# Kernel tuning notes

Hardware: AMD Instinct MI355X
Metric: run time of the kernel (lower is better)

## Reference

```python
import jax, jax.numpy as jnp
import numpy as np

B, H, W = 1, 352, 1216
T = 6          # prop_time
CG = 8         # guidance channels per step
K = 9          # 3x3 propagation kernel


def _conv(x, w, b, pad, groups=1):
    out = jax.lax.conv_general_dilated(
        x, w, (1, 1), [(pad, pad), (pad, pad)],
        dimension_numbers=('NCHW', 'OIHW', 'NCHW'),
        feature_group_count=groups)
    return out if b is None else out + b[None, :, None, None]


def setup_inputs() -> dict:
    key = jax.random.key(0)
    ks = iter(jax.random.split(key, 32))
    def r(shape, s=0.1):
        return jax.random.normal(next(ks), shape, jnp.float32) * s
    return dict(
        feat_init=r((B, 1, H, W), 1.0),
        guidance=r((B, T * CG, H, W), 1.0),
        attn=r((B, 16, H, W), 1.0),
        feat_fix=r((B, 1, H, W), 1.0),
        aff_w_w=r((T, K, CG, 3, 3)), aff_w_b=r((T, K)),
        aff_o_w=r((T, 2 * (K - 1), CG, 3, 3)), aff_o_b=r((T, 2 * (K - 1))),
        proj_w=r((6, 3, 1, 1)),
        bn_gamma=jnp.ones((6,), jnp.float32), bn_beta=jnp.zeros((6,), jnp.float32),
        bn_mean=jnp.zeros((6,), jnp.float32), bn_var=jnp.ones((6,), jnp.float32),
        lsk0_w=r((22, 1, 1, 1)), lsk0_b=r((22,)),
        lsks_w=r((22, 1, 3, 3)), lsks_b=r((22,)),
        lsk1_w=r((11, 22, 1, 1)), lsk1_b=r((11,)),
        lsk2_w=r((11, 22, 1, 1)), lsk2_b=r((11,)),
        lsksq_w=r((2, 2, 3, 3)), lsksq_b=r((2,)),
        lskc_w=r((3, 11, 1, 1)), lskc_b=r((3,)),
    )


def _forward(feat_init, guidance, attn,
             aff_w_w, aff_w_b, aff_o_w, aff_o_b,
             proj_w, bn_gamma, bn_beta, bn_mean, bn_var,
             lsk0_w, lsk0_b, lsks_w, lsks_b, lsk1_w, lsk1_b,
             lsk2_w, lsk2_b, lsksq_w, lsksq_b, lskc_w, lskc_b):
    Bs, _, Hs, Ws = feat_init.shape
    # split guidance into T chunks of CG channels -> (T,B,CG,H,W)
    g = guidance.reshape(Bs, T, CG, Hs, Ws).transpose(1, 0, 2, 3, 4)

    def aff_fn(g_t, ww, wb, ow, ob):
        w = jax.nn.sigmoid(_conv(g_t, ww, wb, 1))              # (B,9,H,W)
        w = w / (w.sum(1, keepdims=True) + 1e-8)
        o = _conv(g_t, ow, ob, 1).reshape(Bs, K - 1, 2, Hs, Ws)
        zero = jnp.zeros((Bs, 1, 2, Hs, Ws), o.dtype)          # reference pixel
        o = jnp.concatenate([o[:, :4], zero, o[:, 4:]], 1).reshape(Bs, 2 * K, Hs, Ws)
        return o, w

    offs, affs = jax.vmap(aff_fn)(g, aff_w_w, aff_w_b, aff_o_w, aff_o_b)

    # modulated deformable conv, weight = ones(1,1,3,3), bias = 0, stride=1, pad=1
    ky = (jnp.repeat(jnp.arange(3), 3) - 1).astype(feat_init.dtype)  # (9,)
    kx = (jnp.tile(jnp.arange(3), 3) - 1).astype(feat_init.dtype)
    yy = jnp.arange(Hs, dtype=feat_init.dtype)
    xx = jnp.arange(Ws, dtype=feat_init.dtype)
    bidx = jnp.arange(Bs)[:, None, None, None]

    def dcn(feat, off, aff):
        img = feat[:, 0]                                       # (B,H,W)
        ys = yy[None, None, :, None] + ky[None, :, None, None] + off[:, 0::2]
        xs = xx[None, None, None, :] + kx[None, :, None, None] + off[:, 1::2]
        y0 = jnp.floor(ys); x0 = jnp.floor(xs)
        wy = ys - y0; wx = xs - x0
        y0i = y0.astype(jnp.int32); x0i = x0.astype(jnp.int32)
        def g4(yi, xi):
            valid = (yi >= 0) & (yi < Hs) & (xi >= 0) & (xi < Ws)
            v = img[bidx, jnp.clip(yi, 0, Hs - 1), jnp.clip(xi, 0, Ws - 1)]
            return v * valid.astype(v.dtype)
        samp = (g4(y0i, x0i) * (1 - wy) * (1 - wx)
                + g4(y0i, x0i + 1) * (1 - wy) * wx
                + g4(y0i + 1, x0i) * wy * (1 - wx)
                + g4(y0i + 1, x0i + 1) * wy * wx)
        return (aff * samp).sum(1)[:, None]                    # (B,1,H,W)

    def step(f, ox):
        o, a = ox
        fn = dcn(f, o, a)
        return fn, fn

    _, feats = jax.lax.scan(step, feat_init.astype(jnp.float32), (offs, affs))

    # combine(list_feat[3:6], attn)
    x3 = jnp.concatenate([feats[3], feats[4], feats[5]], 1)    # (B,3,H,W)
    sf = _conv(x3, proj_w, None, 0)                            # conv 3->6, no bias
    sf = (sf - bn_mean[None, :, None, None]) * jax.lax.rsqrt(bn_var + 1e-5)[None, :, None, None] \
         * bn_gamma[None, :, None, None] + bn_beta[None, :, None, None]
    sf = jnp.where(sf >= 0, sf, 0.2 * sf)                      # LeakyReLU(0.2)
    x22 = jnp.concatenate([attn, sf], 1)                       # (B,22,H,W)

    a1 = _conv(x22, lsk0_w, lsk0_b, 0, 22)                     # depthwise 1x1
    a2 = _conv(a1, lsks_w, lsks_b, 1, 22)                      # depthwise 3x3
    a1 = _conv(a1, lsk1_w, lsk1_b, 0)                          # 22->11
    a2 = _conv(a2, lsk2_w, lsk2_b, 0)                          # 22->11
    cat = jnp.concatenate([a1, a2], 1)
    agg = jnp.concatenate([cat.mean(1, keepdims=True), cat.max(1, keepdims=True)], 1)
    sig = jax.nn.sigmoid(_conv(agg, lsksq_w, lsksq_b, 1))
    at = a1 * sig[:, 0:1] + a2 * sig[:, 1:2]
    at = _conv(at, lskc_w, lskc_b, 0)                          # 11->3
    return (x3 * at).sum(1, keepdims=True)                     # (B,1,H,W)


def reference(feat_init, guidance, attn, feat_fix,
              aff_w_w, aff_w_b, aff_o_w, aff_o_b,
              proj_w, bn_gamma, bn_beta, bn_mean, bn_var,
              lsk0_w, lsk0_b, lsks_w, lsks_b, lsk1_w, lsk1_b,
              lsk2_w, lsk2_b, lsksq_w, lsksq_b, lskc_w, lskc_b):
    # feat_fix only feeds an unused mask path (if False branch) in the original
    return _forward(feat_init, guidance, attn,
                    aff_w_w, aff_w_b, aff_o_w, aff_o_b,
                    proj_w, bn_gamma, bn_beta, bn_mean, bn_var,
                    lsk0_w, lsk0_b, lsks_w, lsks_b, lsk1_w, lsk1_b,
                    lsk2_w, lsk2_b, lsksq_w, lsksq_b, lskc_w, lskc_b)
```

## Files before the change

### kernel.cpp

```cpp
#include <hip/hip_runtime.h>
#include <hip/hip_bf16.h>

#define HH 352
#define WW 1216
#define HWSZ (HH * WW)
#define TT 6

#define WS_CW   16
#define WS_TW   11008
#define WS_FB   12032

typedef __attribute__((ext_vector_type(4))) float f32x4;
typedef __attribute__((ext_vector_type(8))) short s16x8;
union FU { unsigned int u[4]; s16x8 v; };

__device__ inline float ld_in(const void* p, long long i, int bf) {
    return bf ? __bfloat162float(((const __hip_bfloat16*)p)[i]) : ((const float*)p)[i];
}

__device__ inline unsigned int bfsplit_pack(float v) {
    unsigned int uv = __float_as_uint(v);
    unsigned int h = (uv + 0x7FFFu + ((uv >> 16) & 1u)) >> 16;
    float hf = __uint_as_float(h << 16);
    float r = v - hf;
    unsigned int ur = __float_as_uint(r);
    unsigned int l = (ur + 0x7FFFu + ((ur >> 16) & 1u)) >> 16;
    return (h & 0xFFFFu) | (l << 16);
}

__device__ inline int detect_mode(const void* guid) {
    const unsigned int* u = (const unsigned int*)guid;
    int cnt = 0;
    for (int i = 0; i < 128; ++i) {
        unsigned int lo = u[i] & 0xFFFFu;
        int e = (int)((lo >> 7) & 0xFF);
        if (e >= 110 && e <= 140) cnt++;
    }
    return (cnt >= 96) ? 1 : 0;
}

__global__ void prep_small(const void* guid,
                           const void* aww, const void* awb, const void* aow, const void* aob,
                           const void* projw, const void* bng, const void* bnb,
                           const void* bnm, const void* bnv,
                           const void* l0w, const void* l0b, const void* lsw, const void* lsb,
                           const void* l1w, const void* l1b, const void* l2w, const void* l2b,
                           const void* sqw, const void* sqb, const void* lcw, const void* lcb,
                           float* ws) {
    __shared__ int smode;
    if (threadIdx.x == 0) {
        int mode = detect_mode(guid);
        smode = mode;
        if (blockIdx.x == 0) *(int*)ws = mode;
    }
    __syncthreads();
    const int bf = smode;
    const int tid = blockIdx.x * blockDim.x + threadIdx.x;
    const int stp = gridDim.x * blockDim.x;
    float* cw = ws + WS_CW;
    for (int idx = tid; idx < TT * 9 * 72; idx += stp) {
        int t = idx / 648; int r = idx % 648;
        int co = r / 72; int ci = (r % 72) / 9; int tap = r % 9;
        cw[t * 1825 + 25 + co * 72 + ci * 9 + tap] = ld_in(aww, idx, bf);
    }
    for (int idx = tid; idx < TT * 16 * 72; idx += stp) {
        int t = idx / 1152; int r = idx % 1152;
        int co = r / 72; int ci = (r % 72) / 9; int tap = r % 9;
        cw[t * 1825 + 25 + (9 + co) * 72 + ci * 9 + tap] = ld_in(aow, idx, bf);
    }
    for (int idx = tid; idx < TT * 9; idx += stp)
        cw[(idx / 9) * 1825 + (idx % 9)] = ld_in(awb, idx, bf);
    for (int idx = tid; idx < TT * 16; idx += stp)
        cw[(idx / 16) * 1825 + 9 + (idx % 16)] = ld_in(aob, idx, bf);

    float* tw = ws + WS_TW;
    for (int i = tid; i < 18; i += stp) tw[i] = ld_in(projw, i, bf);
    for (int i = tid; i < 6; i += stp) {
        float sc = ld_in(bng, i, bf) * rsqrtf(ld_in(bnv, i, bf) + 1e-5f);
        tw[18 + i] = sc;
        tw[24 + i] = ld_in(bnb, i, bf) - ld_in(bnm, i, bf) * sc;
    }
    for (int i = tid; i < 22;  i += stp) tw[32  + i] = ld_in(l0w, i, bf);
    for (int i = tid; i < 22;  i += stp) tw[54  + i] = ld_in(l0b, i, bf);
    for (int i = tid; i < 198; i += stp) tw[76  + i] = ld_in(lsw, i, bf);
    for (int i = tid; i < 22;  i += stp) tw[274 + i] = ld_in(lsb, i, bf);
    for (int i = tid; i < 242; i += stp) tw[296 + i] = ld_in(l1w, i, bf);
    for (int i = tid; i < 11;  i += stp) tw[538 + i] = ld_in(l1b, i, bf);
    for (int i = tid; i < 242; i += stp) tw[549 + i] = ld_in(l2w, i, bf);
    for (int i = tid; i < 11;  i += stp) tw[791 + i] = ld_in(l2b, i, bf);
    for (int i = tid; i < 36;  i += stp) tw[802 + i] = ld_in(sqw, i, bf);
    for (int i = tid; i < 2;   i += stp) tw[838 + i] = ld_in(sqb, i, bf);
    for (int i = tid; i < 33;  i += stp) tw[840 + i] = ld_in(lcw, i, bf);
    for (int i = tid; i < 3;   i += stp) tw[873 + i] = ld_in(lcb, i, bf);
}

__global__ void prep_feat(const void* __restrict__ feat_init, const int* __restrict__ flagp,
                          float* __restrict__ dst) {
    int bf = *flagp;
    int i = blockIdx.x * 256 + threadIdx.x;
    if (i < HWSZ) dst[i] = ld_in(feat_init, i, bf);
}

__device__ inline float samp(const float* __restrict__ src, int y, int x) {
    bool valid = (y >= 0) & (y < HH) & (x >= 0) & (x < WW);
    int yc = min(max(y, 0), HH - 1);
    int xc = min(max(x, 0), WW - 1);
    float v = src[yc * WW + xc];
    return valid ? v : 0.0f;
}

__global__ __launch_bounds__(256) void dcn_fused(
        const void* __restrict__ guid, const int* __restrict__ flagp,
        const float* __restrict__ wts,
        const float* __restrict__ src, float* __restrict__ dst, int t) {
    __shared__ unsigned int hal[8][10][36];
    __shared__ float outb[4][64][27];
    const int bf = *flagp;
    const int bx = blockIdx.x % 38, by = blockIdx.x / 38;
    const int x0 = bx * 32, y0 = by * 8;
    for (int idx = threadIdx.x; idx < 8 * 360; idx += 256) {
        int ci = idx / 360; int r = (idx % 360) / 36; int c = idx % 36;
        int gy = y0 - 1 + r, gx = x0 - 1 + c;
        float v = 0.f;
        if (c < 34 && gy >= 0 && gy < HH && gx >= 0 && gx < WW)
            v = ld_in(guid, (long long)(t * 8 + ci) * HWSZ + gy * WW + gx, bf);
        hal[ci][r][c] = bfsplit_pack(v);
    }
    const int lane = threadIdx.x & 63;
    const int wave = threadIdx.x >> 6;
    const int col = lane & 15, g = lane >> 4;

    FU Bh[2][3], Bl[2][3];
#pragma unroll
    for (int Nt = 0; Nt < 2; ++Nt)
#pragma unroll
    for (int c = 0; c < 3; ++c) {
        unsigned short eh[8], el[8];
#pragma unroll
        for (int j = 0; j < 8; ++j) {
            int ci = 2 * g + (j >> 2), dx = j & 3;
            int cc = Nt * 16 + col;
            float w = 0.f;
            if (cc < 25 && dx < 3) w = wts[25 + cc * 72 + ci * 9 + c * 3 + dx];
            unsigned int pk = bfsplit_pack(w);
            eh[j] = (unsigned short)(pk & 0xFFFFu);
            el[j] = (unsigned short)(pk >> 16);
        }
#pragma unroll
        for (int q = 0; q < 4; ++q) {
            Bh[Nt][c].u[q] = (unsigned int)eh[2*q] | ((unsigned int)eh[2*q+1] << 16);
            Bl[Nt][c].u[q] = (unsigned int)el[2*q] | ((unsigned int)el[2*q+1] << 16);
        }
    }
    __syncthreads();

    const float* bias = wts;
#pragma unroll
    for (int m = 0; m < 4; ++m) {
        const int M = wave * 4 + m;
        const int py = M >> 1;
        const int pxx = (M & 1) * 16 + col;
        FU Ah[3], Al[3];
#pragma unroll
        for (int c = 0; c < 3; ++c) {
            const unsigned int* r0 = &hal[2 * g][py + c][pxx];
            const unsigned int* r1 = &hal[2 * g + 1][py + c][pxx];
            unsigned int q0 = r0[0], q1 = r0[1], q2 = r0[2], q3 = r0[3];
            unsigned int q4 = r1[0], q5 = r1[1], q6 = r1[2], q7 = r1[3];
            Ah[c].u[0] = __builtin_amdgcn_perm(q1, q0, 0x05040100u);
            Ah[c].u[1] = __builtin_amdgcn_perm(q3, q2, 0x05040100u);
            Ah[c].u[2] = __builtin_amdgcn_perm(q5, q4, 0x05040100u);
            Ah[c].u[3] = __builtin_amdgcn_perm(q7, q6, 0x05040100u);
            Al[c].u[0] = __builtin_amdgcn_perm(q1, q0, 0x07060302u);
            Al[c].u[1] = __builtin_amdgcn_perm(q3, q2, 0x07060302u);
            Al[c].u[2] = __builtin_amdgcn_perm(q5, q4, 0x07060302u);
            Al[c].u[3] = __builtin_amdgcn_perm(q7, q6, 0x07060302u);
        }
#pragma unroll
        for (int Nt = 0; Nt < 2; ++Nt) {
            f32x4 acc = {0.f, 0.f, 0.f, 0.f};
#pragma unroll
            for (int c = 0; c < 3; ++c) {
                acc = __builtin_amdgcn_mfma_f32_16x16x32_bf16(Ah[c].v, Bh[Nt][c].v, acc, 0, 0, 0);
                acc = __builtin_amdgcn_mfma_f32_16x16x32_bf16(Al[c].v, Bh[Nt][c].v, acc, 0, 0, 0);
                acc = __builtin_amdgcn_mfma_f32_16x16x32_bf16(Ah[c].v, Bl[Nt][c].v, acc, 0, 0, 0);
            }
            const int co = Nt * 16 + col;
            if (co < 25) {
                float bs = bias[co];
#pragma unroll
                for (int r = 0; r < 4; ++r)
                    outb[wave][m * 16 + g * 4 + r][co] = acc[r] + bs;
            }
        }
    }
    __syncthreads();
    {
        const int pl = lane;
        const int Ml = pl >> 4, rd = pl & 15;
        const int M = wave * 4 + Ml;
        const int py = M >> 1;
        const int pxx = (M & 1) * 16 + rd;
        const int gy = y0 + py, gx = x0 + pxx;
        float v[25];
#pragma unroll
        for (int c = 0; c < 25; ++c) v[c] = outb[wave][pl][c];
        float w9[9], s = 0.f;
#pragma unroll
        for (int k = 0; k < 9; ++k) { w9[k] = 1.f / (1.f + __expf(-v[k])); s += w9[k]; }
        const float inv = 1.f / (s + 1e-8f);
        float out = 0.f;
#pragma unroll
        for (int k = 0; k < 9; ++k) {
            float oy = 0.f, ox = 0.f;
            if (k != 4) {
                int kp = (k < 4) ? k : (k - 1);
                oy = v[9 + 2 * kp];
                ox = v[10 + 2 * kp];
            }
            float ys = (float)(gy + k / 3 - 1) + oy;
            float xs = (float)(gx + k % 3 - 1) + ox;
            float yf = floorf(ys), xf = floorf(xs);
            float wy = ys - yf, wx = xs - xf;
            int yi = (int)yf, xi = (int)xf;
            float v00 = samp(src, yi, xi);
            float v01 = samp(src, yi, xi + 1);
            float v10 = samp(src, yi + 1, xi);
            float v11 = samp(src, yi + 1, xi + 1);
            float sv = v00 * (1.f - wy) * (1.f - wx) + v01 * (1.f - wy) * wx
                     + v10 * wy * (1.f - wx) + v11 * wy * wx;
            out = fmaf(w9[k] * inv, sv, out);
        }
        dst[gy * WW + gx] = out;
    }
}

__global__ __launch_bounds__(256) void tail1(
        const void* __restrict__ attn, const int* __restrict__ flagp,
        const float* __restrict__ tw, const float* __restrict__ feats,
        float* __restrict__ a1) {
    const int bf = *flagp;
    const int p = blockIdx.x * 256 + threadIdx.x;
    float x3[3] = { feats[3 * HWSZ + p], feats[4 * HWSZ + p], feats[5 * HWSZ + p] };
    float sf[6];
#pragma unroll
    for (int j = 0; j < 6; ++j) {
        float v = tw[j * 3 + 0] * x3[0] + tw[j * 3 + 1] * x3[1] + tw[j * 3 + 2] * x3[2];
        v = v * tw[18 + j] + tw[24 + j];
        sf[j] = (v >= 0.0f) ? v : 0.2f * v;
    }
#pragma unroll
    for (int c = 0; c < 22; ++c) {
        float x = (c < 16) ? ld_in(attn, (long long)c * HWSZ + p, bf) : sf[c - 16];
        a1[c * HWSZ + p] = fmaf(x, tw[32 + c], tw[54 + c]);
    }
}

__global__ __launch_bounds__(256) void tail2(
        const float* __restrict__ tw, const float* __restrict__ a1,
        float* __restrict__ a11, float* __restrict__ a21, float* __restrict__ agg) {
    __shared__ float tile[10][34];
    const int bx = blockIdx.x % 38, by = blockIdx.x / 38;
    const int x0 = bx * 32, y0 = by * 8;
    const int lx = threadIdx.x % 32, ly = threadIdx.x / 32;
    float acc1[11], acc2[11];
#pragma unroll
    for (int j = 0; j < 11; ++j) { acc1[j] = tw[538 + j]; acc2[j] = tw[791 + j]; }
    for (int c = 0; c < 22; ++c) {
        __syncthreads();
        for (int idx = threadIdx.x; idx < 340; idx += 256) {
            int r = idx / 34, cc = idx % 34;
            int gy = y0 - 1 + r, gx = x0 - 1 + cc;
            tile[r][cc] = (gy >= 0 && gy < HH && gx >= 0 && gx < WW)
                          ? a1[c * HWSZ + gy * WW + gx] : 0.0f;
        }
        __syncthreads();
        float a1c = tile[ly + 1][lx + 1];
        float a2c = tw[274 + c];
#pragma unroll
        for (int dy = 0; dy < 3; ++dy)
#pragma unroll
            for (int dx = 0; dx < 3; ++dx)
                a2c = fmaf(tile[ly + dy][lx + dx], tw[76 + c * 9 + dy * 3 + dx], a2c);
#pragma unroll
        for (int j = 0; j < 11; ++j) {
            acc1[j] = fmaf(a1c, tw[296 + j * 22 + c], acc1[j]);
            acc2[j] = fmaf(a2c, tw[549 + j * 22 + c], acc2[j]);
        }
    }
    const int p = (y0 + ly) * WW + x0 + lx;
    float s = 0.0f, mx = -1e30f;
#pragma unroll
    for (int j = 0; j < 11; ++j) {
        a11[j * HWSZ + p] = acc1[j];
        a21[j * HWSZ + p] = acc2[j];
        s += acc1[j] + acc2[j];
        mx = fmaxf(mx, fmaxf(acc1[j], acc2[j]));
    }
    agg[p] = s * (1.0f / 22.0f);
    agg[HWSZ + p] = mx;
}

__global__ __launch_bounds__(256) void tail3(
        const int* __restrict__ flagp, const float* __restrict__ tw,
        const float* __restrict__ feats,
        const float* __restrict__ a11, const float* __restrict__ a21,
        const float* __restrict__ agg, void* __restrict__ out) {
    __shared__ float t0[10][34], t1[10][34];
    const int bx = blockIdx.x % 38, by = blockIdx.x / 38;
    const int x0 = bx * 32, y0 = by * 8;
    for (int idx = threadIdx.x; idx < 340; idx += 256) {
        int r = idx / 34, cc = idx % 34;
        int gy = y0 - 1 + r, gx = x0 - 1 + cc;
        bool ok = (gy >= 0 && gy < HH && gx >= 0 && gx < WW);
        t0[r][cc] = ok ? agg[gy * WW + gx] : 0.0f;
        t1[r][cc] = ok ? agg[HWSZ + gy * WW + gx] : 0.0f;
    }
    __syncthreads();
    const int lx = threadIdx.x % 32, ly = threadIdx.x / 32;
    float s0 = tw[838], s1 = tw[839];
#pragma unroll
    for (int dy = 0; dy < 3; ++dy)
#pragma unroll
        for (int dx = 0; dx < 3; ++dx) {
            float v0 = t0[ly + dy][lx + dx], v1 = t1[ly + dy][lx + dx];
            s0 = fmaf(v0, tw[802 + 0 * 18 + 0 * 9 + dy * 3 + dx], s0);
            s0 = fmaf(v1, tw[802 + 0 * 18 + 1 * 9 + dy * 3 + dx], s0);
            s1 = fmaf(v0, tw[802 + 1 * 18 + 0 * 9 + dy * 3 + dx], s1);
            s1 = fmaf(v1, tw[802 + 1 * 18 + 1 * 9 + dy * 3 + dx], s1);
        }
    float sg0 = 1.0f / (1.0f + __expf(-s0));
    float sg1 = 1.0f / (1.0f + __expf(-s1));
    const int p = (y0 + ly) * WW + x0 + lx;
    float at3[3] = { tw[873], tw[874], tw[875] };
#pragma unroll
    for (int j = 0; j < 11; ++j) {
        float at = a11[j * HWSZ + p] * sg0 + a21[j * HWSZ + p] * sg1;
#pragma unroll
        for (int i = 0; i < 3; ++i) at3[i] = fmaf(at, tw[840 + i * 11 + j], at3[i]);
    }
    float o = feats[3 * HWSZ + p] * at3[0] + feats[4 * HWSZ + p] * at3[1]
            + feats[5 * HWSZ + p] * at3[2];
    int bf = *flagp;
    if (bf) ((__hip_bfloat16*)out)[p] = __float2bfloat16(o);
    else    ((float*)out)[p] = o;
}

extern "C" void kernel_launch(void* const* d_in, const int* in_sizes, int n_in,
                              void* d_out, int out_size, void* d_ws, size_t ws_size,
                              hipStream_t stream) {
    (void)in_sizes; (void)n_in; (void)out_size; (void)ws_size;
    float* WSF = (float*)d_ws;
    const int* flagp = (const int*)d_ws;
    float* cw   = WSF + WS_CW;
    float* tw   = WSF + WS_TW;
    float* FB   = WSF + WS_FB;
    float* A1   = FB + 7 * HWSZ;
    float* A11  = A1 + 22 * HWSZ;
    float* A21  = A11 + 11 * HWSZ;
    float* AGG  = A21 + 11 * HWSZ;

    prep_small<<<32, 256, 0, stream>>>(d_in[1],
        d_in[4], d_in[5], d_in[6], d_in[7],
        d_in[8], d_in[9], d_in[10], d_in[11], d_in[12],
        d_in[13], d_in[14], d_in[15], d_in[16],
        d_in[17], d_in[18], d_in[19], d_in[20],
        d_in[21], d_in[22], d_in[23], d_in[24], WSF);
    prep_feat<<<(HWSZ + 255) / 256, 256, 0, stream>>>(d_in[0], flagp, FB + 6 * HWSZ);

    for (int t = 0; t < 6; ++t) {
        const float* src = (t == 0) ? (FB + 6 * HWSZ) : (FB + (t - 1) * HWSZ);
        dcn_fused<<<44 * 38, 256, 0, stream>>>(d_in[1], flagp, cw + t * 1825, src, FB + t * HWSZ, t);
    }
    tail1<<<HWSZ / 256, 256, 0, stream>>>(d_in[2], flagp, tw, FB, A1);
    tail2<<<44 * 38, 256, 0, stream>>>(tw, A1, A11, A21, AGG);
    tail3<<<44 * 38, 256, 0, stream>>>(flagp, tw, FB, A11, A21, AGG, d_out);
}
```

Measured before the change: 484.4 us.

## Fuse prep kernels, widen DCN to 512 threads, recompute LSK tail in shared memory

Merges the small-weight prep and the feat_init conversion into a single launch. The deformable conv kernel now runs 512 threads per block with one wave per row, and the two half-waves split the nine bilinear taps before combining them with a shuffle. The three tail kernels become two: tailA computes only the mean/max aggregate from a shared-memory tile, and tailB recomputes the 22-channel LSK activations instead of reading the 22+11+11 planes written to global memory earlier. This removes large global intermediates and one launch, at the cost of doing the LSK convolution twice and using more shared memory per block.

```diff
diff --git a/kernel.cpp b/kernel.cpp
--- a/kernel.cpp
+++ b/kernel.cpp
@@ -39,14 +39,15 @@
     return (cnt >= 96) ? 1 : 0;
 }
 
-__global__ void prep_small(const void* guid,
-                           const void* aww, const void* awb, const void* aow, const void* aob,
-                           const void* projw, const void* bng, const void* bnb,
-                           const void* bnm, const void* bnv,
-                           const void* l0w, const void* l0b, const void* lsw, const void* lsb,
-                           const void* l1w, const void* l1b, const void* l2w, const void* l2b,
-                           const void* sqw, const void* sqb, const void* lcw, const void* lcb,
-                           float* ws) {
+__global__ __launch_bounds__(256) void prep_all(
+        const void* feat_init, const void* guid,
+        const void* aww, const void* awb, const void* aow, const void* aob,
+        const void* projw, const void* bng, const void* bnb,
+        const void* bnm, const void* bnv,
+        const void* l0w, const void* l0b, const void* lsw, const void* lsb,
+        const void* l1w, const void* l1b, const void* l2w, const void* l2b,
+        const void* sqw, const void* sqb, const void* lcw, const void* lcb,
+        float* ws) {
     __shared__ int smode;
     if (threadIdx.x == 0) {
         int mode = detect_mode(guid);
@@ -55,8 +56,13 @@
     }
     __syncthreads();
     const int bf = smode;
-    const int tid = blockIdx.x * blockDim.x + threadIdx.x;
-    const int stp = gridDim.x * blockDim.x;
+    {
+        int i = blockIdx.x * 256 + threadIdx.x;
+        if (i < HWSZ) ws[WS_FB + 6 * HWSZ + i] = ld_in(feat_init, i, bf);
+    }
+    if (blockIdx.x >= 32) return;
+    const int tid = blockIdx.x * 256 + threadIdx.x;
+    const int stp = 32 * 256;
     float* cw = ws + WS_CW;
     for (int idx = tid; idx < TT * 9 * 72; idx += stp) {
         int t = idx / 648; int r = idx % 648;
@@ -94,13 +100,6 @@
     for (int i = tid; i < 3;   i += stp) tw[873 + i] = ld_in(lcb, i, bf);
 }
 
-__global__ void prep_feat(const void* __restrict__ feat_init, const int* __restrict__ flagp,
-                          float* __restrict__ dst) {
-    int bf = *flagp;
-    int i = blockIdx.x * 256 + threadIdx.x;
-    if (i < HWSZ) dst[i] = ld_in(feat_init, i, bf);
-}
-
 __device__ inline float samp(const float* __restrict__ src, int y, int x) {
     bool valid = (y >= 0) & (y < HH) & (x >= 0) & (x < WW);
     int yc = min(max(y, 0), HH - 1);
@@ -109,16 +108,16 @@
     return valid ? v : 0.0f;
 }
 
-__global__ __launch_bounds__(256) void dcn_fused(
+__global__ __launch_bounds__(512) void dcn_fused(
         const void* __restrict__ guid, const int* __restrict__ flagp,
         const float* __restrict__ wts,
         const float* __restrict__ src, float* __restrict__ dst, int t) {
     __shared__ unsigned int hal[8][10][36];
-    __shared__ float outb[4][64][27];
+    __shared__ float outb[8][32][26];
     const int bf = *flagp;
     const int bx = blockIdx.x % 38, by = blockIdx.x / 38;
     const int x0 = bx * 32, y0 = by * 8;
-    for (int idx = threadIdx.x; idx < 8 * 360; idx += 256) {
+    for (int idx = threadIdx.x; idx < 8 * 360; idx += 512) {
         int ci = idx / 360; int r = (idx % 360) / 36; int c = idx % 36;
         int gy = y0 - 1 + r, gx = x0 - 1 + c;
         float v = 0.f;
@@ -156,15 +155,13 @@
 
     const float* bias = wts;
 #pragma unroll
-    for (int m = 0; m < 4; ++m) {
-        const int M = wave * 4 + m;
-        const int py = M >> 1;
-        const int pxx = (M & 1) * 16 + col;
+    for (int m = 0; m < 2; ++m) {
+        const int pxx = m * 16 + col;
         FU Ah[3], Al[3];
 #pragma unroll
         for (int c = 0; c < 3; ++c) {
-            const unsigned int* r0 = &hal[2 * g][py + c][pxx];
-            const unsigned int* r1 = &hal[2 * g + 1][py + c][pxx];
+            const unsigned int* r0 = &hal[2 * g][wave + c][pxx];
+            const unsigned int* r1 = &hal[2 * g + 1][wave + c][pxx];
             unsigned int q0 = r0[0], q1 = r0[1], q2 = r0[2], q3 = r0[3];
             unsigned int q4 = r1[0], q5 = r1[1], q6 = r1[2], q7 = r1[3];
             Ah[c].u[0] = __builtin_amdgcn_perm(q1, q0, 0x05040100u);
@@ -194,32 +191,40 @@
             }
         }
     }
-    __syncthreads();
     {
-        const int pl = lane;
-        const int Ml = pl >> 4, rd = pl & 15;
-        const int M = wave * 4 + Ml;
-        const int py = M >> 1;
-        const int pxx = (M & 1) * 16 + rd;
-        const int gy = y0 + py, gx = x0 + pxx;
+        const int half = lane >> 5;
+        const int pxl = lane & 31;
+        const int gy = y0 + wave, gx = x0 + pxl;
         float v[25];
 #pragma unroll
-        for (int c = 0; c < 25; ++c) v[c] = outb[wave][pl][c];
+        for (int c = 0; c < 25; ++c) v[c] = outb[wave][pxl][c];
         float w9[9], s = 0.f;
 #pragma unroll
         for (int k = 0; k < 9; ++k) { w9[k] = 1.f / (1.f + __expf(-v[k])); s += w9[k]; }
         const float inv = 1.f / (s + 1e-8f);
         float out = 0.f;
 #pragma unroll
-        for (int k = 0; k < 9; ++k) {
-            float oy = 0.f, ox = 0.f;
-            if (k != 4) {
-                int kp = (k < 4) ? k : (k - 1);
-                oy = v[9 + 2 * kp];
-                ox = v[10 + 2 * kp];
-            }
-            float ys = (float)(gy + k / 3 - 1) + oy;
-            float xs = (float)(gx + k % 3 - 1) + ox;
+        for (int tp = 0; tp < 5; ++tp) {
+            const int ka = tp;
+            const int kb = tp + 5;
+            const bool vb = (kb < 9);
+            float wa = w9[ka] * inv;
+            float wb = vb ? w9[kb < 9 ? kb : 8] * inv : 0.f;
+            float w  = half ? wb : wa;
+            const int kpa = (ka < 4) ? ka : ka - 1;
+            const int kpb = vb ? ((kb < 4) ? kb : kb - 1) : 0;
+            float oya = (ka == 4) ? 0.f : v[9 + 2 * kpa];
+            float oxa = (ka == 4) ? 0.f : v[10 + 2 * kpa];
+            float oyb = vb ? v[9 + 2 * kpb] : 0.f;
+            float oxb = vb ? v[10 + 2 * kpb] : 0.f;
+            float oy = half ? oyb : oya;
+            float ox = half ? oxb : oxa;
+            const int dya = ka / 3 - 1, dxa = ka % 3 - 1;
+            const int dyb = vb ? kb / 3 - 1 : 0, dxb = vb ? kb % 3 - 1 : 0;
+            int dy = half ? dyb : dya;
+            int dx = half ? dxb : dxa;
+            float ys = (float)(gy + dy) + oy;
+            float xs = (float)(gx + dx) + ox;
             float yf = floorf(ys), xf = floorf(xs);
             float wy = ys - yf, wx = xs - xf;
             int yi = (int)yf, xi = (int)xf;
@@ -229,119 +234,140 @@
             float v11 = samp(src, yi + 1, xi + 1);
             float sv = v00 * (1.f - wy) * (1.f - wx) + v01 * (1.f - wy) * wx
                      + v10 * wy * (1.f - wx) + v11 * wy * wx;
-            out = fmaf(w9[k] * inv, sv, out);
-        }
-        dst[gy * WW + gx] = out;
-    }
-}
-
-__global__ __launch_bounds__(256) void tail1(
-        const void* __restrict__ attn, const int* __restrict__ flagp,
-        const float* __restrict__ tw, const float* __restrict__ feats,
-        float* __restrict__ a1) {
-    const int bf = *flagp;
-    const int p = blockIdx.x * 256 + threadIdx.x;
-    float x3[3] = { feats[3 * HWSZ + p], feats[4 * HWSZ + p], feats[5 * HWSZ + p] };
-    float sf[6];
-#pragma unroll
-    for (int j = 0; j < 6; ++j) {
-        float v = tw[j * 3 + 0] * x3[0] + tw[j * 3 + 1] * x3[1] + tw[j * 3 + 2] * x3[2];
-        v = v * tw[18 + j] + tw[24 + j];
-        sf[j] = (v >= 0.0f) ? v : 0.2f * v;
-    }
-#pragma unroll
-    for (int c = 0; c < 22; ++c) {
-        float x = (c < 16) ? ld_in(attn, (long long)c * HWSZ + p, bf) : sf[c - 16];
-        a1[c * HWSZ + p] = fmaf(x, tw[32 + c], tw[54 + c]);
-    }
-}
-
-__global__ __launch_bounds__(256) void tail2(
-        const float* __restrict__ tw, const float* __restrict__ a1,
-        float* __restrict__ a11, float* __restrict__ a21, float* __restrict__ agg) {
-    __shared__ float tile[10][34];
-    const int bx = blockIdx.x % 38, by = blockIdx.x / 38;
-    const int x0 = bx * 32, y0 = by * 8;
-    const int lx = threadIdx.x % 32, ly = threadIdx.x / 32;
-    float acc1[11], acc2[11];
+            out = fmaf(w, sv, out);
+        }
+        out += __shfl_xor(out, 32);
+        if (half == 0) dst[gy * WW + gx] = out;
+    }
+}
+
+__device__ inline void stage_a1_ft(const void* attn, int bf, const float* tw,
+                                   const float* feats, float (*a1t)[10][34],
+                                   float (*ft)[10][34], int x0, int y0) {
+    for (int idx = threadIdx.x; idx < 19 * 340; idx += 256) {
+        int plane = idx / 340; int r = (idx % 340) / 34; int cc = idx % 34;
+        int gy = y0 - 1 + r, gx = x0 - 1 + cc;
+        bool ok = (gy >= 0 && gy < HH && gx >= 0 && gx < WW);
+        if (plane < 16) {
+            float x = ok ? ld_in(attn, (long long)plane * HWSZ + gy * WW + gx, bf) : 0.f;
+            a1t[plane][r][cc] = ok ? fmaf(x, tw[32 + plane], tw[54 + plane]) : 0.f;
+        } else {
+            ft[plane - 16][r][cc] = ok ? feats[(long long)(3 + plane - 16) * HWSZ + gy * WW + gx] : 0.f;
+        }
+    }
+}
+
+__device__ inline void fill_sf(const float* tw, float (*a1t)[10][34],
+                               const float (*ft)[10][34], int x0, int y0) {
+    for (int idx = threadIdx.x; idx < 6 * 340; idx += 256) {
+        int j = idx / 340; int r = (idx % 340) / 34; int cc = idx % 34;
+        int gy = y0 - 1 + r, gx = x0 - 1 + cc;
+        bool ok = (gy >= 0 && gy < HH && gx >= 0 && gx < WW);
+        float o = 0.f;
+        if (ok) {
+            float f0 = ft[0][r][cc], f1 = ft[1][r][cc], f2 = ft[2][r][cc];
+            float v = tw[j * 3 + 0] * f0 + tw[j * 3 + 1] * f1 + tw[j * 3 + 2] * f2;
+            v = v * tw[18 + j] + tw[24 + j];
+            v = (v >= 0.f) ? v : 0.2f * v;
+            o = fmaf(v, tw[32 + 16 + j], tw[54 + 16 + j]);
+        }
+        a1t[16 + j][r][cc] = o;
+    }
+}
+
+__device__ inline void lsk_acc(const float (*a1t)[10][34], const float* tw,
+                               int lx, int ly, float* acc1, float* acc2) {
 #pragma unroll
     for (int j = 0; j < 11; ++j) { acc1[j] = tw[538 + j]; acc2[j] = tw[791 + j]; }
     for (int c = 0; c < 22; ++c) {
-        __syncthreads();
-        for (int idx = threadIdx.x; idx < 340; idx += 256) {
-            int r = idx / 34, cc = idx % 34;
-            int gy = y0 - 1 + r, gx = x0 - 1 + cc;
-            tile[r][cc] = (gy >= 0 && gy < HH && gx >= 0 && gx < WW)
-                          ? a1[c * HWSZ + gy * WW + gx] : 0.0f;
-        }
-        __syncthreads();
-        float a1c = tile[ly + 1][lx + 1];
+        float a1c = a1t[c][ly + 1][lx + 1];
         float a2c = tw[274 + c];
 #pragma unroll
         for (int dy = 0; dy < 3; ++dy)
 #pragma unroll
-            for (int dx = 0; dx < 3; ++dx)
-                a2c = fmaf(tile[ly + dy][lx + dx], tw[76 + c * 9 + dy * 3 + dx], a2c);
+        for (int dx = 0; dx < 3; ++dx)
+            a2c = fmaf(a1t[c][ly + dy][lx + dx], tw[76 + c * 9 + dy * 3 + dx], a2c);
 #pragma unroll
         for (int j = 0; j < 11; ++j) {
             acc1[j] = fmaf(a1c, tw[296 + j * 22 + c], acc1[j]);
             acc2[j] = fmaf(a2c, tw[549 + j * 22 + c], acc2[j]);
         }
     }
-    const int p = (y0 + ly) * WW + x0 + lx;
-    float s = 0.0f, mx = -1e30f;
+}
+
+__global__ __launch_bounds__(256) void tailA(
+        const void* __restrict__ attn, const int* __restrict__ flagp,
+        const float* __restrict__ tw, const float* __restrict__ feats,
+        float* __restrict__ agg) {
+    __shared__ float a1t[22][10][34];
+    __shared__ float ft[3][10][34];
+    const int bf = *flagp;
+    const int bx = blockIdx.x % 38, by = blockIdx.x / 38;
+    const int x0 = bx * 32, y0 = by * 8;
+    stage_a1_ft(attn, bf, tw, feats, a1t, ft, x0, y0);
+    __syncthreads();
+    fill_sf(tw, a1t, ft, x0, y0);
+    __syncthreads();
+    const int lx = threadIdx.x & 31, ly = threadIdx.x >> 5;
+    float acc1[11], acc2[11];
+    lsk_acc(a1t, tw, lx, ly, acc1, acc2);
+    float s = 0.f, mx = -1e30f;
 #pragma unroll
     for (int j = 0; j < 11; ++j) {
-        a11[j * HWSZ + p] = acc1[j];
-        a21[j * HWSZ + p] = acc2[j];
         s += acc1[j] + acc2[j];
         mx = fmaxf(mx, fmaxf(acc1[j], acc2[j]));
     }
+    const int p = (y0 + ly) * WW + x0 + lx;
     agg[p] = s * (1.0f / 22.0f);
     agg[HWSZ + p] = mx;
 }
 
-__global__ __launch_bounds__(256) void tail3(
-        const int* __restrict__ flagp, const float* __restrict__ tw,
-        const float* __restrict__ feats,
-        const float* __restrict__ a11, const float* __restrict__ a21,
+__global__ __launch_bounds__(256) void tailB(
+        const void* __restrict__ attn, const int* __restrict__ flagp,
+        const float* __restrict__ tw, const float* __restrict__ feats,
         const float* __restrict__ agg, void* __restrict__ out) {
-    __shared__ float t0[10][34], t1[10][34];
+    __shared__ float a1t[22][10][34];
+    __shared__ float ft[3][10][34];
+    __shared__ float gt[2][10][34];
+    const int bf = *flagp;
     const int bx = blockIdx.x % 38, by = blockIdx.x / 38;
     const int x0 = bx * 32, y0 = by * 8;
-    for (int idx = threadIdx.x; idx < 340; idx += 256) {
-        int r = idx / 34, cc = idx % 34;
+    stage_a1_ft(attn, bf, tw, feats, a1t, ft, x0, y0);
+    for (int idx = threadIdx.x; idx < 2 * 340; idx += 256) {
+        int plane = idx / 340; int r = (idx % 340) / 34; int cc = idx % 34;
         int gy = y0 - 1 + r, gx = x0 - 1 + cc;
         bool ok = (gy >= 0 && gy < HH && gx >= 0 && gx < WW);
-        t0[r][cc] = ok ? agg[gy * WW + gx] : 0.0f;
-        t1[r][cc] = ok ? agg[HWSZ + gy * WW + gx] : 0.0f;
-    }
-    __syncthreads();
-    const int lx = threadIdx.x % 32, ly = threadIdx.x / 32;
+        gt[plane][r][cc] = ok ? agg[(long long)plane * HWSZ + gy * WW + gx] : 0.f;
+    }
+    __syncthreads();
+    fill_sf(tw, a1t, ft, x0, y0);
+    __syncthreads();
+    const int lx = threadIdx.x & 31, ly = threadIdx.x >> 5;
+    float acc1[11], acc2[11];
+    lsk_acc(a1t, tw, lx, ly, acc1, acc2);
     float s0 = tw[838], s1 = tw[839];
 #pragma unroll
     for (int dy = 0; dy < 3; ++dy)
 #pragma unroll
-        for (int dx = 0; dx < 3; ++dx) {
-            float v0 = t0[ly + dy][lx + dx], v1 = t1[ly + dy][lx + dx];
-            s0 = fmaf(v0, tw[802 + 0 * 18 + 0 * 9 + dy * 3 + dx], s0);
-            s0 = fmaf(v1, tw[802 + 0 * 18 + 1 * 9 + dy * 3 + dx], s0);
-            s1 = fmaf(v0, tw[802 + 1 * 18 + 0 * 9 + dy * 3 + dx], s1);
-            s1 = fmaf(v1, tw[802 + 1 * 18 + 1 * 9 + dy * 3 + dx], s1);
-        }
+    for (int dx = 0; dx < 3; ++dx) {
+        float v0 = gt[0][ly + dy][lx + dx], v1 = gt[1][ly + dy][lx + dx];
+        s0 = fmaf(v0, tw[802 + 0 * 18 + 0 * 9 + dy * 3 + dx], s0);
+        s0 = fmaf(v1, tw[802 + 0 * 18 + 1 * 9 + dy * 3 + dx], s0);
+        s1 = fmaf(v0, tw[802 + 1 * 18 + 0 * 9 + dy * 3 + dx], s1);
+        s1 = fmaf(v1, tw[802 + 1 * 18 + 1 * 9 + dy * 3 + dx], s1);
+    }
     float sg0 = 1.0f / (1.0f + __expf(-s0));
     float sg1 = 1.0f / (1.0f + __expf(-s1));
+    float at3[3] = { tw[873], tw[874], tw[875] };
+#pragma unroll
+    for (int j = 0; j < 11; ++j) {
+        float at = acc1[j] * sg0 + acc2[j] * sg1;
+#pragma unroll
+        for (int i = 0; i < 3; ++i) at3[i] = fmaf(at, tw[840 + i * 11 + j], at3[i]);
+    }
+    float o = ft[0][ly + 1][lx + 1] * at3[0] + ft[1][ly + 1][lx + 1] * at3[1]
+            + ft[2][ly + 1][lx + 1] * at3[2];
     const int p = (y0 + ly) * WW + x0 + lx;
-    float at3[3] = { tw[873], tw[874], tw[875] };
-#pragma unroll
-    for (int j = 0; j < 11; ++j) {
-        float at = a11[j * HWSZ + p] * sg0 + a21[j * HWSZ + p] * sg1;
-#pragma unroll
-        for (int i = 0; i < 3; ++i) at3[i] = fmaf(at, tw[840 + i * 11 + j], at3[i]);
-    }
-    float o = feats[3 * HWSZ + p] * at3[0] + feats[4 * HWSZ + p] * at3[1]
-            + feats[5 * HWSZ + p] * at3[2];
-    int bf = *flagp;
     if (bf) ((__hip_bfloat16*)out)[p] = __float2bfloat16(o);
     else    ((float*)out)[p] = o;
 }
@@ -355,24 +381,19 @@
     float* cw   = WSF + WS_CW;
     float* tw   = WSF + WS_TW;
     float* FB   = WSF + WS_FB;
-    float* A1   = FB + 7 * HWSZ;
-    float* A11  = A1 + 22 * HWSZ;
-    float* A21  = A11 + 11 * HWSZ;
-    float* AGG  = A21 + 11 * HWSZ;
-
-    prep_small<<<32, 256, 0, stream>>>(d_in[1],
+    float* AGG  = FB + 7 * HWSZ;
+
+    prep_all<<<1672, 256, 0, stream>>>(d_in[0], d_in[1],
         d_in[4], d_in[5], d_in[6], d_in[7],
         d_in[8], d_in[9], d_in[10], d_in[11], d_in[12],
         d_in[13], d_in[14], d_in[15], d_in[16],
         d_in[17], d_in[18], d_in[19], d_in[20],
         d_in[21], d_in[22], d_in[23], d_in[24], WSF);
-    prep_feat<<<(HWSZ + 255) / 256, 256, 0, stream>>>(d_in[0], flagp, FB + 6 * HWSZ);
 
     for (int t = 0; t < 6; ++t) {
         const float* src = (t == 0) ? (FB + 6 * HWSZ) : (FB + (t - 1) * HWSZ);
-        dcn_fused<<<44 * 38, 256, 0, stream>>>(d_in[1], flagp, cw + t * 1825, src, FB + t * HWSZ, t);
-    }
-    tail1<<<HWSZ / 256, 256, 0, stream>>>(d_in[2], flagp, tw, FB, A1);
-    tail2<<<44 * 38, 256, 0, stream>>>(tw, A1, A11, A21, AGG);
-    tail3<<<44 * 38, 256, 0, stream>>>(flagp, tw, FB, A11, A21, AGG, d_out);
-}
+        dcn_fused<<<44 * 38, 512, 0, stream>>>(d_in[1], flagp, cw + t * 1825, src, FB + t * HWSZ, t);
+    }
+    tailA<<<44 * 38, 256, 0, stream>>>(d_in[2], flagp, tw, FB, AGG);
+    tailB<<<44 * 38, 256, 0, stream>>>(d_in[2], flagp, tw, FB, AGG, d_out);
+}
```

Measured after the change: 587.6 us. 1.21x slower.
